# Optimization experiments

Measured on AMD Instinct MI355X. Metric: run time of the kernel, lower is better.

## Reference

```python
import jax, jax.numpy as jnp
import numpy as np

NOISE_EPS = 0.01
LB_COEFF = 0.01
TOP_K = 2


def setup_inputs() -> dict:
    key = jax.random.key(0)
    k1, k2, k3 = jax.random.split(key, 3)
    B, S, H, E = 4, 4096, 4096, 8
    x = jax.random.normal(k1, (B, S, H), dtype=jnp.float32)
    W = jax.random.normal(k2, (H, E), dtype=jnp.float32) * (1.0 / np.sqrt(H))
    b = jnp.zeros((E,), dtype=jnp.float32)
    noise = jax.random.normal(k3, (B * S, E), dtype=jnp.float32)
    return {"x": x, "W": W, "b": b, "noise": noise}


def reference(x, W, b, noise):
    B, S, H = x.shape
    E = W.shape[1]
    x_flat = x.reshape(-1, H)                      # [BS, H]
    logits = x_flat @ W + b + noise * NOISE_EPS    # [BS, E]
    routing_weights = jax.nn.softmax(logits, axis=-1)
    top_k_weights, top_k_indices = jax.lax.top_k(routing_weights, TOP_K)
    top_k_weights = top_k_weights / jnp.sum(top_k_weights, axis=-1, keepdims=True)
    # load-balancing aux loss
    expert_usage = jnp.mean(routing_weights, axis=0)        # [E]
    target = 1.0 / E
    aux_loss = LB_COEFF * jnp.sum((expert_usage - target) ** 2)
    return (top_k_weights.reshape(B, S, TOP_K),
            top_k_indices.reshape(B, S, TOP_K),
            aux_loss)
```

## Files before the change

kernel.cpp:

```cpp
#include <hip/hip_runtime.h>


#define BS      16384
#define HDIM    4096
#define NE      8
#define RPW     4
#define NWAVE   16
#define NITER   16
#define NOISE_EPS 0.01f
#define LB_COEFF  0.01f

__global__ __launch_bounds__(1024, 4)
void router_main(const float* __restrict__ x, const float* __restrict__ W,
                 const float* __restrict__ bias, const float* __restrict__ noise,
                 float* __restrict__ out, float* __restrict__ part) {
    const int tid  = threadIdx.x;
    const int lane = tid & 63;
    const int wave = tid >> 6;
    const int row0 = blockIdx.x * (NWAVE * RPW) + wave * RPW;

    __shared__ float4 w_lds[HDIM * 2];
    __shared__ float block_usage[NE];
    if (tid < NE) block_usage[tid] = 0.0f;
    {
        const float4* __restrict__ W4 = (const float4*)W;
        for (int i = tid; i < HDIM * 2; i += 1024) {
            const int f = i >> 3, j = i & 7;
            w_lds[(i & ~7) | (j ^ (f & 7))] = W4[i];
        }
    }
    __syncthreads();

    float acc[RPW][NE];
#pragma unroll
    for (int r = 0; r < RPW; ++r)
#pragma unroll
        for (int e = 0; e < NE; ++e) acc[r][e] = 0.0f;

    const float4* __restrict__ x4 = (const float4*)x + (size_t)row0 * (HDIM / 4);
    const int wxor = lane & 7;

    float4 bufA[RPW], bufB[RPW], bufC[RPW];

#define CHUNKC(k) (((k) + wave) & 15)

#define LOADTO(BUF, k)                                                        \
    {                                                                         \
        const int o_ = CHUNKC(k) * 64 + lane;                                 \
        _Pragma("unroll")                                                     \
        for (int r = 0; r < RPW; ++r)                                         \
            BUF[r] = x4[r * (HDIM / 4) + o_];                                 \
    }

#define FMA_HALF(XC, F, KK)                                                   \
    {                                                                         \
        float4 wr[4];                                                         \
        _Pragma("unroll")                                                     \
        for (int m = 0; m < 4; ++m)                                           \
            wr[m] = w_lds[(F) * 8 + ((4 * (KK) + m) ^ wxor)];                 \
        _Pragma("unroll")                                                     \
        for (int r = 0; r < RPW; ++r) {                                       \
            _Pragma("unroll")                                                 \
            for (int kq = 0; kq < 2; ++kq) {                                  \
                const int k = 2 * (KK) + kq;                                  \
                const float xv = ((const float*)&XC[r])[k];                   \
                acc[r][0] += xv * wr[2 * kq].x;                               \
                acc[r][1] += xv * wr[2 * kq].y;                               \
                acc[r][2] += xv * wr[2 * kq].z;                               \
                acc[r][3] += xv * wr[2 * kq].w;                               \
                acc[r][4] += xv * wr[2 * kq + 1].x;                           \
                acc[r][5] += xv * wr[2 * kq + 1].y;                           \
                acc[r][6] += xv * wr[2 * kq + 1].z;                           \
                acc[r][7] += xv * wr[2 * kq + 1].w;                           \
            }                                                                 \
        }                                                                     \
    }

#define BODY(BUF, k)                                                          \
    {                                                                         \
        const int F_ = CHUNKC(k) * 64 + lane;                                 \
        FMA_HALF(BUF, F_, 0)                                                  \
        FMA_HALF(BUF, F_, 1)                                                  \
    }

    LOADTO(bufA, 0)
    LOADTO(bufB, 1)
    LOADTO(bufC, 2)

#pragma unroll 1
    for (int s = 0; s < 4; ++s) {
        const int k0 = 3 * s;
        BODY(bufA, k0)     LOADTO(bufA, k0 + 3)
        BODY(bufB, k0 + 1) LOADTO(bufB, k0 + 4)
        BODY(bufC, k0 + 2) LOADTO(bufC, k0 + 5)
    }
    BODY(bufA, 12) LOADTO(bufA, 15)
    BODY(bufB, 13)
    BODY(bufC, 14)
    BODY(bufA, 15)

#undef BODY
#undef FMA_HALF
#undef LOADTO
#undef CHUNKC

#pragma unroll
    for (int r = 0; r < RPW; ++r)
#pragma unroll
        for (int e = 0; e < NE; ++e) {
            float v = acc[r][e];
#pragma unroll
            for (int m = 1; m < 64; m <<= 1) v += __shfl_xor(v, m, 64);
            acc[r][e] = v;
        }

    if (lane < RPW) {
        const int row = row0 + lane;

        float logits[NE];
#pragma unroll
        for (int r = 0; r < RPW; ++r)
            if (lane == r)
#pragma unroll
                for (int e = 0; e < NE; ++e) logits[e] = acc[r][e];

        const float4 b_lo = ((const float4*)bias)[0];
        const float4 b_hi = ((const float4*)bias)[1];
        const float4 n_lo = ((const float4*)(noise + (size_t)row * NE))[0];
        const float4 n_hi = ((const float4*)(noise + (size_t)row * NE))[1];

        logits[0] += b_lo.x + NOISE_EPS * n_lo.x;
        logits[1] += b_lo.y + NOISE_EPS * n_lo.y;
        logits[2] += b_lo.z + NOISE_EPS * n_lo.z;
        logits[3] += b_lo.w + NOISE_EPS * n_lo.w;
        logits[4] += b_hi.x + NOISE_EPS * n_hi.x;
        logits[5] += b_hi.y + NOISE_EPS * n_hi.y;
        logits[6] += b_hi.z + NOISE_EPS * n_hi.z;
        logits[7] += b_hi.w + NOISE_EPS * n_hi.w;

        float m = logits[0];
#pragma unroll
        for (int e = 1; e < NE; ++e) m = fmaxf(m, logits[e]);
        float p[NE], s = 0.0f;
#pragma unroll
        for (int e = 0; e < NE; ++e) { p[e] = expf(logits[e] - m); s += p[e]; }
        const float inv_s = 1.0f / s;

        float v1 = p[0]; int e1 = 0;
#pragma unroll
        for (int e = 1; e < NE; ++e) if (p[e] > v1) { v1 = p[e]; e1 = e; }
        float v2 = -1.0f; int e2 = 0;
#pragma unroll
        for (int e = 0; e < NE; ++e)
            if (e != e1 && p[e] > v2) { v2 = p[e]; e2 = e; }

        const float inv_d = 1.0f / (v1 + v2);
        out[(size_t)row * 2]     = v1 * inv_d;
        out[(size_t)row * 2 + 1] = v2 * inv_d;
        out[(size_t)(BS * 2) + row * 2]     = (float)e1;
        out[(size_t)(BS * 2) + row * 2 + 1] = (float)e2;

#pragma unroll
        for (int e = 0; e < NE; ++e)
            atomicAdd(&block_usage[e], p[e] * inv_s);
    }

    __syncthreads();
    if (tid < NE) part[blockIdx.x * NE + tid] = block_usage[tid];
}

__global__ void router_finalize(const float* __restrict__ part,
                                float* __restrict__ out) {
    const int lane = threadIdx.x & 63;
    float p[NE];
#pragma unroll
    for (int e = 0; e < NE; ++e) p[e] = 0.0f;
#pragma unroll
    for (int j = 0; j < 4; ++j) {
        const int b = lane * 4 + j;
#pragma unroll
        for (int e = 0; e < NE; ++e) p[e] += part[b * NE + e];
    }
#pragma unroll
    for (int e = 0; e < NE; ++e) {
        float v = p[e];
#pragma unroll
        for (int m = 1; m < 64; m <<= 1) v += __shfl_xor(v, m, 64);
        p[e] = v;
    }
    if (lane == 0) {
        float aux = 0.0f;
#pragma unroll
        for (int e = 0; e < NE; ++e) {
            const float mean = p[e] * (1.0f / (float)BS);
            const float d = mean - (1.0f / (float)NE);
            aux += d * d;
        }
        out[(size_t)BS * 4] = LB_COEFF * aux;
    }
}

extern "C" void kernel_launch(void* const* d_in, const int* in_sizes, int n_in,
                              void* d_out, int out_size, void* d_ws, size_t ws_size,
                              hipStream_t stream) {
    const float* x     = (const float*)d_in[0];
    const float* W     = (const float*)d_in[1];
    const float* b     = (const float*)d_in[2];
    const float* noise = (const float*)d_in[3];
    float* out  = (float*)d_out;
    float* part = (float*)d_ws;

    const int blocks = BS / (NWAVE * RPW);
    router_main<<<blocks, 1024, 0, stream>>>(x, W, b, noise, out, part);
    router_finalize<<<1, 64, 0, stream>>>(part, out);
}
```

Baseline: 392.4 us.

## Assign one row per wave instead of four and launch four times more blocks

Each wave now computes the routing logits for a single row, dropping the 4-row register blocking and the staggered chunk order. The grid grows to one block per 16 rows, and the finalize kernel sums the larger set of per-block partials. The intent is lower register pressure and more parallelism. In exchange, each W element read from LDS serves one row instead of four, and W is staged into LDS by four times as many blocks.

```diff
diff --git a/kernel.cpp b/kernel.cpp
--- a/kernel.cpp
+++ b/kernel.cpp
@@ -4,9 +4,7 @@
 #define BS      16384
 #define HDIM    4096
 #define NE      8
-#define RPW     4
 #define NWAVE   16
-#define NITER   16
 #define NOISE_EPS 0.01f
 #define LB_COEFF  0.01f
 
@@ -17,7 +15,7 @@
     const int tid  = threadIdx.x;
     const int lane = tid & 63;
     const int wave = tid >> 6;
-    const int row0 = blockIdx.x * (NWAVE * RPW) + wave * RPW;
+    const int row  = blockIdx.x * NWAVE + wave;
 
     __shared__ float4 w_lds[HDIM * 2];
     __shared__ float block_usage[NE];
@@ -31,98 +29,71 @@
     }
     __syncthreads();
 
-    float acc[RPW][NE];
+    float acc[NE];
 #pragma unroll
-    for (int r = 0; r < RPW; ++r)
-#pragma unroll
-        for (int e = 0; e < NE; ++e) acc[r][e] = 0.0f;
+    for (int e = 0; e < NE; ++e) acc[e] = 0.0f;
 
-    const float4* __restrict__ x4 = (const float4*)x + (size_t)row0 * (HDIM / 4);
+    const float4* __restrict__ x4 = (const float4*)x + (size_t)row * (HDIM / 4);
     const int wxor = lane & 7;
 
-    float4 bufA[RPW], bufB[RPW], bufC[RPW];
+    float4 b0, b1, b2, b3;
 
-#define CHUNKC(k) (((k) + wave) & 15)
+#define LOADTO(B, k) B = x4[(k) * 64 + lane];
 
-#define LOADTO(BUF, k)                                                        \
+#define BODY(B, k)                                                            \
     {                                                                         \
-        const int o_ = CHUNKC(k) * 64 + lane;                                 \
+        const int F_ = (k) * 64 + lane;                                       \
+        float4 wr[8];                                                         \
         _Pragma("unroll")                                                     \
-        for (int r = 0; r < RPW; ++r)                                         \
-            BUF[r] = x4[r * (HDIM / 4) + o_];                                 \
-    }
-
-#define FMA_HALF(XC, F, KK)                                                   \
-    {                                                                         \
-        float4 wr[4];                                                         \
+        for (int m = 0; m < 8; ++m)                                           \
+            wr[m] = w_lds[F_ * 8 + (m ^ wxor)];                               \
         _Pragma("unroll")                                                     \
-        for (int m = 0; m < 4; ++m)                                           \
-            wr[m] = w_lds[(F) * 8 + ((4 * (KK) + m) ^ wxor)];                 \
-        _Pragma("unroll")                                                     \
-        for (int r = 0; r < RPW; ++r) {                                       \
-            _Pragma("unroll")                                                 \
-            for (int kq = 0; kq < 2; ++kq) {                                  \
-                const int k = 2 * (KK) + kq;                                  \
-                const float xv = ((const float*)&XC[r])[k];                   \
-                acc[r][0] += xv * wr[2 * kq].x;                               \
-                acc[r][1] += xv * wr[2 * kq].y;                               \
-                acc[r][2] += xv * wr[2 * kq].z;                               \
-                acc[r][3] += xv * wr[2 * kq].w;                               \
-                acc[r][4] += xv * wr[2 * kq + 1].x;                           \
-                acc[r][5] += xv * wr[2 * kq + 1].y;                           \
-                acc[r][6] += xv * wr[2 * kq + 1].z;                           \
-                acc[r][7] += xv * wr[2 * kq + 1].w;                           \
-            }                                                                 \
+        for (int k4 = 0; k4 < 4; ++k4) {                                      \
+            const float xv = ((const float*)&B)[k4];                          \
+            acc[0] += xv * wr[2 * k4].x;                                      \
+            acc[1] += xv * wr[2 * k4].y;                                      \
+            acc[2] += xv * wr[2 * k4].z;                                      \
+            acc[3] += xv * wr[2 * k4].w;                                      \
+            acc[4] += xv * wr[2 * k4 + 1].x;                                  \
+            acc[5] += xv * wr[2 * k4 + 1].y;                                  \
+            acc[6] += xv * wr[2 * k4 + 1].z;                                  \
+            acc[7] += xv * wr[2 * k4 + 1].w;                                  \
         }                                                                     \
     }
 
-#define BODY(BUF, k)                                                          \
-    {                                                                         \
-        const int F_ = CHUNKC(k) * 64 + lane;                                 \
-        FMA_HALF(BUF, F_, 0)                                                  \
-        FMA_HALF(BUF, F_, 1)                                                  \
+    LOADTO(b0, 0)
+    LOADTO(b1, 1)
+    LOADTO(b2, 2)
+    LOADTO(b3, 3)
+
+#pragma unroll 1
+    for (int s = 0; s < 3; ++s) {
+        const int k0 = 4 * s;
+        BODY(b0, k0)     LOADTO(b0, k0 + 4)
+        BODY(b1, k0 + 1) LOADTO(b1, k0 + 5)
+        BODY(b2, k0 + 2) LOADTO(b2, k0 + 6)
+        BODY(b3, k0 + 3) LOADTO(b3, k0 + 7)
+    }
+    BODY(b0, 12)
+    BODY(b1, 13)
+    BODY(b2, 14)
+    BODY(b3, 15)
+
+#undef BODY
+#undef LOADTO
+
+#pragma unroll
+    for (int e = 0; e < NE; ++e) {
+        float v = acc[e];
+#pragma unroll
+        for (int m = 1; m < 64; m <<= 1) v += __shfl_xor(v, m, 64);
+        acc[e] = v;
     }
 
-    LOADTO(bufA, 0)
-    LOADTO(bufB, 1)
-    LOADTO(bufC, 2)
-
-#pragma unroll 1
-    for (int s = 0; s < 4; ++s) {
-        const int k0 = 3 * s;
-        BODY(bufA, k0)     LOADTO(bufA, k0 + 3)
-        BODY(bufB, k0 + 1) LOADTO(bufB, k0 + 4)
-        BODY(bufC, k0 + 2) LOADTO(bufC, k0 + 5)
-    }
-    BODY(bufA, 12) LOADTO(bufA, 15)
-    BODY(bufB, 13)
-    BODY(bufC, 14)
-    BODY(bufA, 15)
-
-#undef BODY
-#undef FMA_HALF
-#undef LOADTO
-#undef CHUNKC
-
-#pragma unroll
-    for (int r = 0; r < RPW; ++r)
-#pragma unroll
-        for (int e = 0; e < NE; ++e) {
-            float v = acc[r][e];
-#pragma unroll
-            for (int m = 1; m < 64; m <<= 1) v += __shfl_xor(v, m, 64);
-            acc[r][e] = v;
-        }
-
-    if (lane < RPW) {
-        const int row = row0 + lane;
-
+    if (lane == 0) {
         float logits[NE];
 #pragma unroll
-        for (int r = 0; r < RPW; ++r)
-            if (lane == r)
-#pragma unroll
-                for (int e = 0; e < NE; ++e) logits[e] = acc[r][e];
+        for (int e = 0; e < NE; ++e) logits[e] = acc[e];
 
         const float4 b_lo = ((const float4*)bias)[0];
         const float4 b_hi = ((const float4*)bias)[1];
@@ -175,9 +146,8 @@
     float p[NE];
 #pragma unroll
     for (int e = 0; e < NE; ++e) p[e] = 0.0f;
-#pragma unroll
-    for (int j = 0; j < 4; ++j) {
-        const int b = lane * 4 + j;
+    for (int j = 0; j < 16; ++j) {
+        const int b = j * 64 + lane;
 #pragma unroll
         for (int e = 0; e < NE; ++e) p[e] += part[b * NE + e];
     }
@@ -210,7 +180,7 @@
     float* out  = (float*)d_out;
     float* part = (float*)d_ws;
 
-    const int blocks = BS / (NWAVE * RPW);
+    const int blocks = BS / NWAVE;
     router_main<<<blocks, 1024, 0, stream>>>(x, W, b, noise, out, part);
     router_finalize<<<1, 64, 0, stream>>>(part, out);
 }
```

New measurement: 369.3 us. -5.9%, faster.
